# Optimization experiments

Hardware: AMD Instinct MI355X
Metric: run time of the kernel (lower is better)

## Reference

```python
import jax, jax.numpy as jnp
import numpy as np

TAU = 1.0
NUM_NEURONS = 32768
INPUT_SIZE = 8192
BATCH = 512


def setup_inputs() -> dict:
    key = jax.random.key(0)
    k1, k2, k3 = jax.random.split(key, 3)
    x = jax.random.uniform(k1, (BATCH, INPUT_SIZE), dtype=jnp.float32)
    gate_weights = jax.random.normal(k2, (NUM_NEURONS, 16), dtype=jnp.float32)
    input_idx = jax.random.randint(k3, (NUM_NEURONS, 2), 0, INPUT_SIZE, dtype=jnp.int32)
    return {"x": x, "gate_weights": gate_weights, "input_idx": input_idx}


def _all_logic_ops(a, b):
    # 16 soft (real-valued) binary logic gates, stacked on last axis.
    ab = a * b
    one = jnp.ones_like(a)
    zero = jnp.zeros_like(a)
    return jnp.stack([
        zero,                  # FALSE
        ab,                    # a AND b
        a - ab,                # a AND NOT b
        a,                     # a
        b - ab,                # NOT a AND b
        b,                     # b
        a + b - 2.0 * ab,      # a XOR b
        a + b - ab,            # a OR b
        1.0 - (a + b - ab),    # NOR
        1.0 - (a + b - 2.0 * ab),  # XNOR
        1.0 - b,               # NOT b
        1.0 - b + ab,          # a OR NOT b
        1.0 - a,               # NOT a
        1.0 - a + ab,          # NOT a OR b
        1.0 - ab,              # NAND
        one,                   # TRUE
    ], axis=-1)  # (B, N, 16)


def reference(x, gate_weights, input_idx):
    # gather the two input columns per neuron: (B, N)
    a = x[:, input_idx[:, 0]]
    b = x[:, input_idx[:, 1]]
    ops = _all_logic_ops(a, b)                          # (B, N, 16)
    w = jax.nn.softmax(gate_weights / TAU, axis=1)      # (N, 16)
    out = jnp.einsum('bnk,nk->bn', ops, w)              # (B, N)
    return out
```

## Files before the change

kernel.cpp:

```cpp
#include <hip/hip_runtime.h>
#include <hip/hip_bf16.h>

#define NUM_NEURONS 32768
#define INPUT_SIZE  8192
#define BATCH       512

typedef float f32x4 __attribute__((ext_vector_type(4)));

__global__ __launch_bounds__(256) void logic_coeff_kernel(
    const float* __restrict__ gw, float4* __restrict__ coeffs)
{
    const int n = blockIdx.x * 256 + threadIdx.x;
    if (n >= NUM_NEURONS) return;
    const float* g = gw + (size_t)n * 16;

    float w[16];
#pragma unroll
    for (int i = 0; i < 16; i += 4) {
        float4 v = *reinterpret_cast<const float4*>(g + i);
        w[i+0] = v.x; w[i+1] = v.y; w[i+2] = v.z; w[i+3] = v.w;
    }
    float m = w[0];
#pragma unroll
    for (int i = 1; i < 16; ++i) m = fmaxf(m, w[i]);
    float s = 0.f;
#pragma unroll
    for (int i = 0; i < 16; ++i) { w[i] = __expf(w[i] - m); s += w[i]; }
    const float inv = 1.0f / s;

    const float C0  = (w[8] + w[9] + w[10] + w[11] + w[12] + w[13] + w[14] + w[15]) * inv;
    const float Ca  = (w[2] + w[3] + w[6] + w[7] - w[8] - w[9] - w[12] - w[13]) * inv;
    const float Cb  = (w[4] + w[5] + w[6] + w[7] - w[8] - w[9] - w[10] - w[11]) * inv;
    const float Cab = (w[1] - w[2] - w[4] - 2.f*w[6] - w[7]
                       + w[8] + 2.f*w[9] + w[11] + w[13] - w[14]) * inv;

    coeffs[n] = make_float4(C0, Ca, Cb, Cab);
}

constexpr int BLK  = 512;
constexpr int RPB  = 2;
constexpr int HALF = NUM_NEURONS / 2;
constexpr int QPT  = HALF / 4 / BLK;
constexpr int SF4  = RPB * INPUT_SIZE / 4 / BLK;

__global__ __launch_bounds__(BLK, 4) void logic_main_kernel(
    const float*  __restrict__ x,
    const float4* __restrict__ coeffs,
    const int4*   __restrict__ idx4,
    float*        __restrict__ out)
{
    __shared__ float sx[RPB][INPUT_SIZE];

    const int tid  = threadIdx.x;
    const int bid  = blockIdx.x;
    const int rp   = bid & 255;
    const int half = bid >> 8;
    const int row0 = rp * RPB;
    const int nh0  = half * HALF;

    {
        const float4* xr = reinterpret_cast<const float4*>(x + (size_t)row0 * INPUT_SIZE);
        float4* s4 = reinterpret_cast<float4*>(&sx[0][0]);
#pragma unroll
        for (int i = 0; i < SF4; ++i) {
            __builtin_amdgcn_global_load_lds(
                (const __attribute__((address_space(1))) void*)(xr + i * BLK + tid),
                (__attribute__((address_space(3))) void*)(s4 + i * BLK + tid),
                16, 0, 0);
        }
    }
    asm volatile("s_waitcnt vmcnt(0)" ::: "memory");
    __builtin_amdgcn_s_barrier();

    const int wid  = tid >> 6;
    const int lane = tid & 63;

    float* o0 = out + (size_t)row0 * NUM_NEURONS;
    float* o1 = o0 + NUM_NEURONS;

#pragma unroll 2
    for (int it = 0; it < QPT; ++it) {
        const int g  = (it + wid) & (QPT - 1);
        const int nb = nh0 + g * 2048 + wid * 256 + lane * 4;

        const float4 c0 = coeffs[nb + 0];
        const float4 c1 = coeffs[nb + 1];
        const float4 c2 = coeffs[nb + 2];
        const float4 c3 = coeffs[nb + 3];
        const int4   p0 = idx4[(nb >> 1) + 0];
        const int4   p1 = idx4[(nb >> 1) + 1];

        {
            const float* s = sx[0];
            f32x4 res;
            { const float a = s[p0.x], b = s[p0.y];
              res[0] = fmaf(a, fmaf(c0.w, b, c0.y), fmaf(c0.z, b, c0.x)); }
            { const float a = s[p0.z], b = s[p0.w];
              res[1] = fmaf(a, fmaf(c1.w, b, c1.y), fmaf(c1.z, b, c1.x)); }
            { const float a = s[p1.x], b = s[p1.y];
              res[2] = fmaf(a, fmaf(c2.w, b, c2.y), fmaf(c2.z, b, c2.x)); }
            { const float a = s[p1.z], b = s[p1.w];
              res[3] = fmaf(a, fmaf(c3.w, b, c3.y), fmaf(c3.z, b, c3.x)); }
            __builtin_nontemporal_store(res, reinterpret_cast<f32x4*>(o0 + nb));
        }
        {
            const float* s = sx[1];
            f32x4 res;
            { const float a = s[p0.x], b = s[p0.y];
              res[0] = fmaf(a, fmaf(c0.w, b, c0.y), fmaf(c0.z, b, c0.x)); }
            { const float a = s[p0.z], b = s[p0.w];
              res[1] = fmaf(a, fmaf(c1.w, b, c1.y), fmaf(c1.z, b, c1.x)); }
            { const float a = s[p1.x], b = s[p1.y];
              res[2] = fmaf(a, fmaf(c2.w, b, c2.y), fmaf(c2.z, b, c2.x)); }
            { const float a = s[p1.z], b = s[p1.w];
              res[3] = fmaf(a, fmaf(c3.w, b, c3.y), fmaf(c3.z, b, c3.x)); }
            __builtin_nontemporal_store(res, reinterpret_cast<f32x4*>(o1 + nb));
        }
    }
}

extern "C" void kernel_launch(void* const* d_in, const int* in_sizes, int n_in,
                              void* d_out, int out_size, void* d_ws, size_t ws_size,
                              hipStream_t stream)
{
    const float* x   = (const float*)d_in[0];
    const float* gw  = (const float*)d_in[1];
    const int4*  idx = (const int4*)d_in[2];
    float* out = (float*)d_out;

    float4* coeffs = (float4*)d_ws;

    logic_coeff_kernel<<<NUM_NEURONS / 256, 256, 0, stream>>>(gw, coeffs);

    logic_main_kernel<<<(BATCH / RPB) * 2, BLK, 0, stream>>>(x, coeffs, idx, out);
}
```

Before: 92.45 us.

## Interleave two batch rows in LDS and prefetch coefficients one iteration ahead

The two batch rows in shared memory are interleaved in 128-float chunks, so a neuron's values for both rows sit at offsets d and d+128 and one index computation serves both rows. The main loop now software-pipelines the coefficient and index loads, double-buffering them in registers for the next iteration, and the first loads are issued before the LDS barrier so they overlap the x staging. The loop is fully unrolled. This aims to hide global load latency and cut address arithmetic, at the cost of more registers under the 4-blocks-per-CU launch bound.

```diff
diff --git a/kernel.cpp b/kernel.cpp
--- a/kernel.cpp
+++ b/kernel.cpp
@@ -49,7 +49,7 @@
     const int4*   __restrict__ idx4,
     float*        __restrict__ out)
 {
-    __shared__ float sx[RPB][INPUT_SIZE];
+    __shared__ float sx[RPB * INPUT_SIZE];
 
     const int tid  = threadIdx.x;
     const int bid  = blockIdx.x;
@@ -57,65 +57,73 @@
     const int half = bid >> 8;
     const int row0 = rp * RPB;
     const int nh0  = half * HALF;
+    const int wid  = tid >> 6;
+    const int lane = tid & 63;
 
     {
-        const float4* xr = reinterpret_cast<const float4*>(x + (size_t)row0 * INPUT_SIZE);
-        float4* s4 = reinterpret_cast<float4*>(&sx[0][0]);
+        const float4* xr0 = reinterpret_cast<const float4*>(x + (size_t)row0 * INPUT_SIZE);
+        const float4* xr1 = reinterpret_cast<const float4*>(x + (size_t)(row0 + 1) * INPUT_SIZE);
+        float4* s4 = reinterpret_cast<float4*>(sx);
 #pragma unroll
-        for (int i = 0; i < SF4; ++i) {
+        for (int s = 0; s < SF4; ++s) {
+            const float4* src = ((lane < 32) ? xr0 : xr1) + 32 * (8 * s + wid) + (lane & 31);
             __builtin_amdgcn_global_load_lds(
-                (const __attribute__((address_space(1))) void*)(xr + i * BLK + tid),
-                (__attribute__((address_space(3))) void*)(s4 + i * BLK + tid),
+                (const __attribute__((address_space(1))) void*)src,
+                (__attribute__((address_space(3))) void*)(s4 + 512 * s + tid),
                 16, 0, 0);
         }
     }
+
+    float4 c[2][4];
+    int4   p[2][2];
+    {
+        const int g  = wid & (QPT - 1);
+        const int nb = nh0 + g * 2048 + wid * 256 + lane * 4;
+#pragma unroll
+        for (int j = 0; j < 4; ++j) c[0][j] = coeffs[nb + j];
+        p[0][0] = idx4[(nb >> 1) + 0];
+        p[0][1] = idx4[(nb >> 1) + 1];
+    }
+
     asm volatile("s_waitcnt vmcnt(0)" ::: "memory");
     __builtin_amdgcn_s_barrier();
-
-    const int wid  = tid >> 6;
-    const int lane = tid & 63;
 
     float* o0 = out + (size_t)row0 * NUM_NEURONS;
     float* o1 = o0 + NUM_NEURONS;
 
-#pragma unroll 2
+#pragma unroll
     for (int it = 0; it < QPT; ++it) {
+        const int cur = it & 1;
+
+        if (it + 1 < QPT) {
+            const int gn  = (it + 1 + wid) & (QPT - 1);
+            const int nbn = nh0 + gn * 2048 + wid * 256 + lane * 4;
+#pragma unroll
+            for (int j = 0; j < 4; ++j) c[cur ^ 1][j] = coeffs[nbn + j];
+            p[cur ^ 1][0] = idx4[(nbn >> 1) + 0];
+            p[cur ^ 1][1] = idx4[(nbn >> 1) + 1];
+        }
+
         const int g  = (it + wid) & (QPT - 1);
         const int nb = nh0 + g * 2048 + wid * 256 + lane * 4;
 
-        const float4 c0 = coeffs[nb + 0];
-        const float4 c1 = coeffs[nb + 1];
-        const float4 c2 = coeffs[nb + 2];
-        const float4 c3 = coeffs[nb + 3];
-        const int4   p0 = idx4[(nb >> 1) + 0];
-        const int4   p1 = idx4[(nb >> 1) + 1];
-
-        {
-            const float* s = sx[0];
-            f32x4 res;
-            { const float a = s[p0.x], b = s[p0.y];
-              res[0] = fmaf(a, fmaf(c0.w, b, c0.y), fmaf(c0.z, b, c0.x)); }
-            { const float a = s[p0.z], b = s[p0.w];
-              res[1] = fmaf(a, fmaf(c1.w, b, c1.y), fmaf(c1.z, b, c1.x)); }
-            { const float a = s[p1.x], b = s[p1.y];
-              res[2] = fmaf(a, fmaf(c2.w, b, c2.y), fmaf(c2.z, b, c2.x)); }
-            { const float a = s[p1.z], b = s[p1.w];
-              res[3] = fmaf(a, fmaf(c3.w, b, c3.y), fmaf(c3.z, b, c3.x)); }
-            __builtin_nontemporal_store(res, reinterpret_cast<f32x4*>(o0 + nb));
+        f32x4 r0, r1;
+#pragma unroll
+        for (int j = 0; j < 4; ++j) {
+            const int ia = (j < 2) ? ((j == 0) ? p[cur][0].x : p[cur][0].z)
+                                   : ((j == 2) ? p[cur][1].x : p[cur][1].z);
+            const int ib = (j < 2) ? ((j == 0) ? p[cur][0].y : p[cur][0].w)
+                                   : ((j == 2) ? p[cur][1].y : p[cur][1].w);
+            const int da = (ia & 127) + ((ia >> 7) << 8);
+            const int db = (ib & 127) + ((ib >> 7) << 8);
+            const float a0 = sx[da], a1 = sx[da + 128];
+            const float b0 = sx[db], b1 = sx[db + 128];
+            const float4 cc = c[cur][j];
+            r0[j] = fmaf(a0, fmaf(cc.w, b0, cc.y), fmaf(cc.z, b0, cc.x));
+            r1[j] = fmaf(a1, fmaf(cc.w, b1, cc.y), fmaf(cc.z, b1, cc.x));
         }
-        {
-            const float* s = sx[1];
-            f32x4 res;
-            { const float a = s[p0.x], b = s[p0.y];
-              res[0] = fmaf(a, fmaf(c0.w, b, c0.y), fmaf(c0.z, b, c0.x)); }
-            { const float a = s[p0.z], b = s[p0.w];
-              res[1] = fmaf(a, fmaf(c1.w, b, c1.y), fmaf(c1.z, b, c1.x)); }
-            { const float a = s[p1.x], b = s[p1.y];
-              res[2] = fmaf(a, fmaf(c2.w, b, c2.y), fmaf(c2.z, b, c2.x)); }
-            { const float a = s[p1.z], b = s[p1.w];
-              res[3] = fmaf(a, fmaf(c3.w, b, c3.y), fmaf(c3.z, b, c3.x)); }
-            __builtin_nontemporal_store(res, reinterpret_cast<f32x4*>(o1 + nb));
-        }
+        __builtin_nontemporal_store(r0, reinterpret_cast<f32x4*>(o0 + nb));
+        __builtin_nontemporal_store(r1, reinterpret_cast<f32x4*>(o1 + nb));
     }
 }
 
```

After: 94.43 us. 1.02x slower.

## Pack two batch rows as bf16 pairs in LDS and split neurons into quarters

Applied to the files above, without the earlier changes.

Converts the two staged x rows to bf16 and interleaves them into one 32-bit LDS word per input column. Each gather then fetches both rows' operands in a single LDS read, and the shared-memory footprint is halved, which allows 8 blocks per CU and a grid of 1024 blocks over neuron quarters. The x load now goes through registers instead of the direct global-to-LDS path. The change loses input precision (bf16 rounding of x, about 3 significant digits) and each block reloads x for its quarter.

```diff
diff --git a/kernel.cpp b/kernel.cpp
--- a/kernel.cpp
+++ b/kernel.cpp
@@ -39,49 +39,52 @@
 
 constexpr int BLK  = 512;
 constexpr int RPB  = 2;
-constexpr int HALF = NUM_NEURONS / 2;
-constexpr int QPT  = HALF / 4 / BLK;
-constexpr int SF4  = RPB * INPUT_SIZE / 4 / BLK;
+constexpr int QRT  = NUM_NEURONS / 4;
+constexpr int QPT  = QRT / 4 / BLK;
+constexpr int SEGS = INPUT_SIZE / 4 / BLK;
 
-__global__ __launch_bounds__(BLK, 4) void logic_main_kernel(
+__global__ __launch_bounds__(BLK, 8) void logic_main_kernel(
     const float*  __restrict__ x,
     const float4* __restrict__ coeffs,
     const int4*   __restrict__ idx4,
     float*        __restrict__ out)
 {
-    __shared__ float sx[RPB][INPUT_SIZE];
+    __shared__ unsigned int sx[INPUT_SIZE];
 
     const int tid  = threadIdx.x;
     const int bid  = blockIdx.x;
     const int rp   = bid & 255;
-    const int half = bid >> 8;
+    const int q    = bid >> 8;
     const int row0 = rp * RPB;
-    const int nh0  = half * HALF;
+    const int nq0  = q * QRT;
+    const int wid  = tid >> 6;
+    const int lane = tid & 63;
 
     {
-        const float4* xr = reinterpret_cast<const float4*>(x + (size_t)row0 * INPUT_SIZE);
-        float4* s4 = reinterpret_cast<float4*>(&sx[0][0]);
+        const float* xr0 = x + (size_t)row0 * INPUT_SIZE;
+        const float* xr1 = xr0 + INPUT_SIZE;
 #pragma unroll
-        for (int i = 0; i < SF4; ++i) {
-            __builtin_amdgcn_global_load_lds(
-                (const __attribute__((address_space(1))) void*)(xr + i * BLK + tid),
-                (__attribute__((address_space(3))) void*)(s4 + i * BLK + tid),
-                16, 0, 0);
+        for (int s = 0; s < SEGS; ++s) {
+            const int e = (s * BLK + tid) * 4;
+            const float4 v0 = *reinterpret_cast<const float4*>(xr0 + e);
+            const float4 v1 = *reinterpret_cast<const float4*>(xr1 + e);
+            uint4 pk;
+            asm("v_cvt_pk_bf16_f32 %0, %1, %2" : "=v"(pk.x) : "v"(v0.x), "v"(v1.x));
+            asm("v_cvt_pk_bf16_f32 %0, %1, %2" : "=v"(pk.y) : "v"(v0.y), "v"(v1.y));
+            asm("v_cvt_pk_bf16_f32 %0, %1, %2" : "=v"(pk.z) : "v"(v0.z), "v"(v1.z));
+            asm("v_cvt_pk_bf16_f32 %0, %1, %2" : "=v"(pk.w) : "v"(v0.w), "v"(v1.w));
+            *reinterpret_cast<uint4*>(&sx[e]) = pk;
         }
     }
-    asm volatile("s_waitcnt vmcnt(0)" ::: "memory");
-    __builtin_amdgcn_s_barrier();
-
-    const int wid  = tid >> 6;
-    const int lane = tid & 63;
+    __syncthreads();
 
     float* o0 = out + (size_t)row0 * NUM_NEURONS;
     float* o1 = o0 + NUM_NEURONS;
 
-#pragma unroll 2
+#pragma unroll
     for (int it = 0; it < QPT; ++it) {
         const int g  = (it + wid) & (QPT - 1);
-        const int nb = nh0 + g * 2048 + wid * 256 + lane * 4;
+        const int nb = nq0 + g * 2048 + wid * 256 + lane * 4;
 
         const float4 c0 = coeffs[nb + 0];
         const float4 c1 = coeffs[nb + 1];
@@ -90,32 +93,31 @@
         const int4   p0 = idx4[(nb >> 1) + 0];
         const int4   p1 = idx4[(nb >> 1) + 1];
 
-        {
-            const float* s = sx[0];
-            f32x4 res;
-            { const float a = s[p0.x], b = s[p0.y];
-              res[0] = fmaf(a, fmaf(c0.w, b, c0.y), fmaf(c0.z, b, c0.x)); }
-            { const float a = s[p0.z], b = s[p0.w];
-              res[1] = fmaf(a, fmaf(c1.w, b, c1.y), fmaf(c1.z, b, c1.x)); }
-            { const float a = s[p1.x], b = s[p1.y];
-              res[2] = fmaf(a, fmaf(c2.w, b, c2.y), fmaf(c2.z, b, c2.x)); }
-            { const float a = s[p1.z], b = s[p1.w];
-              res[3] = fmaf(a, fmaf(c3.w, b, c3.y), fmaf(c3.z, b, c3.x)); }
-            __builtin_nontemporal_store(res, reinterpret_cast<f32x4*>(o0 + nb));
-        }
-        {
-            const float* s = sx[1];
-            f32x4 res;
-            { const float a = s[p0.x], b = s[p0.y];
-              res[0] = fmaf(a, fmaf(c0.w, b, c0.y), fmaf(c0.z, b, c0.x)); }
-            { const float a = s[p0.z], b = s[p0.w];
-              res[1] = fmaf(a, fmaf(c1.w, b, c1.y), fmaf(c1.z, b, c1.x)); }
-            { const float a = s[p1.x], b = s[p1.y];
-              res[2] = fmaf(a, fmaf(c2.w, b, c2.y), fmaf(c2.z, b, c2.x)); }
-            { const float a = s[p1.z], b = s[p1.w];
-              res[3] = fmaf(a, fmaf(c3.w, b, c3.y), fmaf(c3.z, b, c3.x)); }
-            __builtin_nontemporal_store(res, reinterpret_cast<f32x4*>(o1 + nb));
-        }
+        const unsigned int va0 = sx[p0.x], vb0 = sx[p0.y];
+        const unsigned int va1 = sx[p0.z], vb1 = sx[p0.w];
+        const unsigned int va2 = sx[p1.x], vb2 = sx[p1.y];
+        const unsigned int va3 = sx[p1.z], vb3 = sx[p1.w];
+
+        f32x4 r0, r1;
+        { const float a = __uint_as_float(va0 << 16), b = __uint_as_float(vb0 << 16);
+          r0[0] = fmaf(a, fmaf(c0.w, b, c0.y), fmaf(c0.z, b, c0.x)); }
+        { const float a = __uint_as_float(va0 & 0xFFFF0000u), b = __uint_as_float(vb0 & 0xFFFF0000u);
+          r1[0] = fmaf(a, fmaf(c0.w, b, c0.y), fmaf(c0.z, b, c0.x)); }
+        { const float a = __uint_as_float(va1 << 16), b = __uint_as_float(vb1 << 16);
+          r0[1] = fmaf(a, fmaf(c1.w, b, c1.y), fmaf(c1.z, b, c1.x)); }
+        { const float a = __uint_as_float(va1 & 0xFFFF0000u), b = __uint_as_float(vb1 & 0xFFFF0000u);
+          r1[1] = fmaf(a, fmaf(c1.w, b, c1.y), fmaf(c1.z, b, c1.x)); }
+        { const float a = __uint_as_float(va2 << 16), b = __uint_as_float(vb2 << 16);
+          r0[2] = fmaf(a, fmaf(c2.w, b, c2.y), fmaf(c2.z, b, c2.x)); }
+        { const float a = __uint_as_float(va2 & 0xFFFF0000u), b = __uint_as_float(vb2 & 0xFFFF0000u);
+          r1[2] = fmaf(a, fmaf(c2.w, b, c2.y), fmaf(c2.z, b, c2.x)); }
+        { const float a = __uint_as_float(va3 << 16), b = __uint_as_float(vb3 << 16);
+          r0[3] = fmaf(a, fmaf(c3.w, b, c3.y), fmaf(c3.z, b, c3.x)); }
+        { const float a = __uint_as_float(va3 & 0xFFFF0000u), b = __uint_as_float(vb3 & 0xFFFF0000u);
+          r1[3] = fmaf(a, fmaf(c3.w, b, c3.y), fmaf(c3.z, b, c3.x)); }
+
+        __builtin_nontemporal_store(r0, reinterpret_cast<f32x4*>(o0 + nb));
+        __builtin_nontemporal_store(r1, reinterpret_cast<f32x4*>(o1 + nb));
     }
 }
 
@@ -132,5 +134,5 @@
 
     logic_coeff_kernel<<<NUM_NEURONS / 256, 256, 0, stream>>>(gw, coeffs);
 
-    logic_main_kernel<<<(BATCH / RPB) * 2, BLK, 0, stream>>>(x, coeffs, idx, out);
+    logic_main_kernel<<<(BATCH / RPB) * 4, BLK, 0, stream>>>(x, coeffs, idx, out);
 }
```

Result: slower. 113.6 us (+22.8%).
